# Optimization experiments

Hardware: AMD Instinct MI355X
Metric: run time of the kernel (lower is better)

## Reference

```python
import jax, jax.numpy as jnp
import numpy as np

EMBED = 1024
HIDDEN = 64  # embed_size // n_heads
B, L = 8, 4096


def setup_inputs() -> dict:
    key = jax.random.key(0)
    k1, k2, k3, k4, k5, k6, k7 = jax.random.split(key, 7)
    query = jax.random.normal(k1, (B, L, EMBED), dtype=jnp.float32)
    key_t = jax.random.normal(k2, (B, L, EMBED), dtype=jnp.float32)
    value = jax.random.normal(k3, (B, L, EMBED), dtype=jnp.float32)
    mask = jax.random.randint(k4, (B, L, L), 0, 2).astype(jnp.bool_)
    # nn.Linear(embed, hidden, bias=False) weights have shape (hidden, embed)
    s = 1.0 / np.sqrt(EMBED)
    WQ = jax.random.uniform(k5, (HIDDEN, EMBED), jnp.float32, -s, s)
    WK = jax.random.uniform(k6, (HIDDEN, EMBED), jnp.float32, -s, s)
    WV = jax.random.uniform(k7, (HIDDEN, EMBED), jnp.float32, -s, s)
    return {"query": query, "key": key_t, "value": value, "mask": mask,
            "WQ": WQ, "WK": WK, "WV": WV}


def reference(query, key, value, mask, WQ, WK, WV):
    # Projections: y = x @ W.T  (Linear without bias)
    Q = jnp.einsum('ble,he->blh', query, WQ)   # [B,L,H]
    K = jnp.einsum('ble,he->blh', key, WK)
    V = jnp.einsum('ble,he->blh', value, WV)
    scale = 1.0 / jnp.sqrt(jnp.asarray(Q.shape[-1], Q.dtype))
    scores = jnp.einsum('bqh,bkh->bqk', Q, K) * scale   # [B,L,L]
    scores = jnp.where(mask, -jnp.inf, scores)
    attn = jax.nn.softmax(scores, axis=-1)
    # dropout p=0.0 -> identity
    return jnp.einsum('bqk,bkh->bqh', attn, V)           # [B,L,H]
```

## Files before the change

### kernel.cpp

```cpp
#include <hip/hip_runtime.h>
#include <hip/hip_bf16.h>

#define NB 8
#define LL 4096
#define EE 1024
#define HH 64

typedef unsigned short u16;
typedef unsigned char u8;
typedef unsigned int u32;
typedef unsigned long long u64;
using bf16x8 = __attribute__((ext_vector_type(8))) short;
using f32x4  = __attribute__((ext_vector_type(4))) float;

__device__ __forceinline__ short f2bf(float f) {
    __hip_bfloat16 h = __float2bfloat16(f);
    return __builtin_bit_cast(short, h);
}

__device__ __forceinline__ bf16x8 pack8(const float4 a, const float4 b) {
    bf16x8 r;
    r[0] = f2bf(a.x); r[1] = f2bf(a.y); r[2] = f2bf(a.z); r[3] = f2bf(a.w);
    r[4] = f2bf(b.x); r[5] = f2bf(b.y); r[6] = f2bf(b.z); r[7] = f2bf(b.w);
    return r;
}

__global__ __launch_bounds__(256) void proj_kernel(
    const float* __restrict__ Xq, const float* __restrict__ Xk, const float* __restrict__ Xv,
    const float* __restrict__ Wq, const float* __restrict__ Wk, const float* __restrict__ Wv,
    u16* __restrict__ Oq, u16* __restrict__ Ok, u16* __restrict__ Ovt)
{
    __shared__ u16 Xs[2][64][72];
    __shared__ u16 Ws2[2][64][72];

    const int which = blockIdx.y;
    const float* X = (which == 0) ? Xq : (which == 1) ? Xk : Xv;
    const float* W = (which == 0) ? Wq : (which == 1) ? Wk : Wv;
    const float scale = (which == 0) ? 0.125f : 1.0f;

    const int tid  = threadIdx.x;
    const int lane = tid & 63;
    const int w    = tid >> 6;
    const int g    = lane >> 4;
    const int c    = lane & 15;
    const int m0   = blockIdx.x * 64;
    const int r    = tid >> 2;
    const int cb   = (tid & 3) * 16;

    const float* xrow = X + (size_t)(m0 + r) * EE + cb;
    const float* wrow = W + (size_t)r * EE + cb;

    float4 xr[4], wr[4];
    #pragma unroll
    for (int i = 0; i < 4; ++i) {
        xr[i] = reinterpret_cast<const float4*>(xrow)[i];
        wr[i] = reinterpret_cast<const float4*>(wrow)[i];
    }
    *reinterpret_cast<bf16x8*>(&Xs[0][r][cb])      = pack8(xr[0], xr[1]);
    *reinterpret_cast<bf16x8*>(&Xs[0][r][cb + 8])  = pack8(xr[2], xr[3]);
    *reinterpret_cast<bf16x8*>(&Ws2[0][r][cb])     = pack8(wr[0], wr[1]);
    *reinterpret_cast<bf16x8*>(&Ws2[0][r][cb + 8]) = pack8(wr[2], wr[3]);
    __syncthreads();

    f32x4 acc[4];
    #pragma unroll
    for (int t = 0; t < 4; ++t) acc[t] = (f32x4){0.f, 0.f, 0.f, 0.f};

    for (int s = 0; s < 16; ++s) {
        const int curb = s & 1, nxtb = curb ^ 1;
        if (s < 15) {
            #pragma unroll
            for (int i = 0; i < 4; ++i) {
                xr[i] = reinterpret_cast<const float4*>(xrow + (s + 1) * 64)[i];
                wr[i] = reinterpret_cast<const float4*>(wrow + (s + 1) * 64)[i];
            }
        }
        __builtin_amdgcn_s_setprio(1);
        #pragma unroll
        for (int kk = 0; kk < 2; ++kk) {
            bf16x8 a = *reinterpret_cast<const bf16x8*>(&Xs[curb][16*w + c][kk*32 + 8*g]);
            #pragma unroll
            for (int t = 0; t < 4; ++t) {
                bf16x8 bb = *reinterpret_cast<const bf16x8*>(&Ws2[curb][16*t + c][kk*32 + 8*g]);
                acc[t] = __builtin_amdgcn_mfma_f32_16x16x32_bf16(a, bb, acc[t], 0, 0, 0);
            }
        }
        __builtin_amdgcn_s_setprio(0);
        if (s < 15) {
            *reinterpret_cast<bf16x8*>(&Xs[nxtb][r][cb])      = pack8(xr[0], xr[1]);
            *reinterpret_cast<bf16x8*>(&Xs[nxtb][r][cb + 8])  = pack8(xr[2], xr[3]);
            *reinterpret_cast<bf16x8*>(&Ws2[nxtb][r][cb])     = pack8(wr[0], wr[1]);
            *reinterpret_cast<bf16x8*>(&Ws2[nxtb][r][cb + 8]) = pack8(wr[2], wr[3]);
        }
        __syncthreads();
    }

    if (which < 2) {
        u16* O = (which == 0) ? Oq : Ok;
        #pragma unroll
        for (int t = 0; t < 4; ++t)
            #pragma unroll
            for (int q = 0; q < 4; ++q) {
                const int mrow = m0 + 16*w + 4*g + q;
                O[(size_t)mrow * HH + 16*t + c] = (u16)f2bf(acc[t][q] * scale);
            }
    } else {
        const int bidx = m0 >> 12;
        #pragma unroll
        for (int t = 0; t < 4; ++t)
            #pragma unroll
            for (int q = 0; q < 4; ++q) {
                const int l = (m0 & (LL - 1)) + 16*w + 4*g + q;
                Ovt[((size_t)bidx * HH + 16*t + c) * LL + l] = (u16)f2bf(acc[t][q]);
            }
    }
}

__global__ __launch_bounds__(256) void attn_kernel(
    const u16* __restrict__ Qb, const u16* __restrict__ Kb, const u16* __restrict__ Vt,
    const int* __restrict__ mask, float* __restrict__ out)
{
    __shared__ u16 Ks[2][64][72];
    __shared__ u16 Vts[2][64][72];
    __shared__ u16 Ps[4][16][72];
    __shared__ u64 Pnl[2][4][64];

    const int b    = blockIdx.x & 7;
    const int q0   = (blockIdx.x >> 3) * 64;
    const int tid  = threadIdx.x;
    const int lane = tid & 63;
    const int w    = tid >> 6;
    const int g    = lane >> 4;
    const int c    = lane & 15;
    const int r    = tid >> 2;
    const int cb   = (tid & 3) * 16;
    const int mrr  = tid >> 4;
    const int mcc  = tid & 15;

    const u16* kbase = Kb + (size_t)b * LL * HH;
    const u16* vbase = Vt + (size_t)b * HH * LL;
    const int* mbase0 = mask + (size_t)b * LL * LL + (size_t)(q0 + mrr) * LL + mcc * 16;

    bf16x8 qf[2];
    {
        const u16* qp = Qb + ((size_t)b * LL + q0 + 16*w + c) * HH;
        qf[0] = *reinterpret_cast<const bf16x8*>(qp + 8*g);
        qf[1] = *reinterpret_cast<const bf16x8*>(qp + 32 + 8*g);
    }

    bf16x8 kra, krb, vra, vrb;
    int4 mA0, mA1, mA2, mA3, mB0, mB1, mB2, mB3;

    #define LOADKV(kt_) do {                                                   \
        kra = *reinterpret_cast<const bf16x8*>(kbase + (size_t)((kt_)*64 + r) * HH + cb);       \
        krb = *reinterpret_cast<const bf16x8*>(kbase + (size_t)((kt_)*64 + r) * HH + cb + 8);   \
        vra = *reinterpret_cast<const bf16x8*>(vbase + (size_t)r * LL + (kt_)*64 + cb);         \
        vrb = *reinterpret_cast<const bf16x8*>(vbase + (size_t)r * LL + (kt_)*64 + cb + 8);     \
    } while (0)
    #define WRITEKV(buf_) do {                                                 \
        *reinterpret_cast<bf16x8*>(&Ks[buf_][r][cb])      = kra;               \
        *reinterpret_cast<bf16x8*>(&Ks[buf_][r][cb + 8])  = krb;               \
        *reinterpret_cast<bf16x8*>(&Vts[buf_][r][cb])     = vra;               \
        *reinterpret_cast<bf16x8*>(&Vts[buf_][r][cb + 8]) = vrb;               \
    } while (0)
    #define MLOADX(P0, P1, P2, P3, sg) do {                                    \
        const int4* _mp = reinterpret_cast<const int4*>(                       \
            mbase0 + (size_t)(16 * ((sg) & 3)) * LL + ((sg) >> 2) * 256);      \
        P0 = _mp[0]; P1 = _mp[1]; P2 = _mp[2]; P3 = _mp[3];                    \
    } while (0)
    #define MPACKX(P0, P1, P2, P3, sg) do {                                    \
        u32 _bb =  (u32)(P0.x != 0)        | ((u32)(P0.y != 0) << 1)           \
                | ((u32)(P0.z != 0) << 2)  | ((u32)(P0.w != 0) << 3)           \
                | ((u32)(P1.x != 0) << 4)  | ((u32)(P1.y != 0) << 5)           \
                | ((u32)(P1.z != 0) << 6)  | ((u32)(P1.w != 0) << 7)           \
                | ((u32)(P2.x != 0) << 8)  | ((u32)(P2.y != 0) << 9)           \
                | ((u32)(P2.z != 0) << 10) | ((u32)(P2.w != 0) << 11)          \
                | ((u32)(P3.x != 0) << 12) | ((u32)(P3.y != 0) << 13)          \
                | ((u32)(P3.z != 0) << 14) | ((u32)(P3.w != 0) << 15);         \
        ((u16*)&Pnl[((sg) >> 2) & 1][mcc >> 2][16 * ((sg) & 3) + mrr])[mcc & 3] = (u16)_bb; \
    } while (0)

    f32x4 acc[4];
    float lpart[4];
    #pragma unroll
    for (int t = 0; t < 4; ++t) acc[t] = (f32x4){0.f, 0.f, 0.f, 0.f};
    #pragma unroll
    for (int q = 0; q < 4; ++q) lpart[q] = 0.f;

    #define TILE_BODY(CUR, PB, TI) do {                                        \
        f32x4 s[4];                                                            \
        __builtin_amdgcn_s_setprio(1);                                         \
        _Pragma("unroll")                                                      \
        for (int t = 0; t < 4; ++t) {                                          \
            s[t] = (f32x4){0.f, 0.f, 0.f, 0.f};                                \
            _Pragma("unroll")                                                  \
            for (int kk = 0; kk < 2; ++kk) {                                   \
                bf16x8 bfr = *reinterpret_cast<const bf16x8*>(&Ks[CUR][16*t + c][kk*32 + 8*g]); \
                s[t] = __builtin_amdgcn_mfma_f32_16x16x32_bf16(qf[kk], bfr, s[t], 0, 0, 0);     \
            }                                                                  \
        }                                                                      \
        __builtin_amdgcn_s_setprio(0);                                         \
        u64 mw0 = Pnl[PB][TI][16*w + 4*g + 0];                                 \
        u64 mw1 = Pnl[PB][TI][16*w + 4*g + 1];                                 \
        u64 mw2 = Pnl[PB][TI][16*w + 4*g + 2];                                 \
        u64 mw3 = Pnl[PB][TI][16*w + 4*g + 3];                                 \
        u32 mlo[4], mhi[4];                                                    \
        mlo[0] = (u32)mw0; mhi[0] = (u32)(mw0 >> 32);                          \
        mlo[1] = (u32)mw1; mhi[1] = (u32)(mw1 >> 32);                          \
        mlo[2] = (u32)mw2; mhi[2] = (u32)(mw2 >> 32);                          \
        mlo[3] = (u32)mw3; mhi[3] = (u32)(mw3 >> 32);                          \
        _Pragma("unroll")                                                      \
        for (int t = 0; t < 4; ++t)                                            \
            _Pragma("unroll")                                                  \
            for (int q = 0; q < 4; ++q) {                                      \
                u32 wsel = (t < 2) ? mlo[q] : mhi[q];                          \
                u32 bit = (wsel >> ((t & 1) * 16 + c)) & 1u;                   \
                float p = bit ? 0.f : __expf(s[t][q]);                         \
                lpart[q] += p;                                                 \
                Ps[w][4*g + q][16*t + c] = (u16)f2bf(p);                       \
            }                                                                  \
        __builtin_amdgcn_s_setprio(1);                                         \
        _Pragma("unroll")                                                      \
        for (int kk = 0; kk < 2; ++kk) {                                       \
            bf16x8 pa = *reinterpret_cast<const bf16x8*>(&Ps[w][c][kk*32 + 8*g]);               \
            _Pragma("unroll")                                                  \
            for (int t = 0; t < 4; ++t) {                                      \
                bf16x8 vfr = *reinterpret_cast<const bf16x8*>(&Vts[CUR][16*t + c][kk*32 + 8*g]);\
                acc[t] = __builtin_amdgcn_mfma_f32_16x16x32_bf16(pa, vfr, acc[t], 0, 0, 0);     \
            }                                                                  \
        }                                                                      \
        __builtin_amdgcn_s_setprio(0);                                         \
    } while (0)

    LOADKV(0);
    MLOADX(mA0, mA1, mA2, mA3, 0); MPACKX(mA0, mA1, mA2, mA3, 0);
    MLOADX(mA0, mA1, mA2, mA3, 1); MPACKX(mA0, mA1, mA2, mA3, 1);
    MLOADX(mA0, mA1, mA2, mA3, 2); MPACKX(mA0, mA1, mA2, mA3, 2);
    MLOADX(mA0, mA1, mA2, mA3, 3); MPACKX(mA0, mA1, mA2, mA3, 3);
    MLOADX(mB0, mB1, mB2, mB3, 4);
    WRITEKV(0);
    __syncthreads();

    for (int it = 0; it < 32; ++it) {
        const int f0 = 2 * it;
        const int f1 = f0 + 1;

        LOADKV(f0 + 1);
        if (f0 <= 58) MLOADX(mA0, mA1, mA2, mA3, f0 + 5);
        TILE_BODY(0, (f0 >> 2) & 1, f0 & 3);
        WRITEKV(1);
        if (f0 <= 59) MPACKX(mB0, mB1, mB2, mB3, f0 + 4);
        __syncthreads();

        if (f1 <= 62) LOADKV(f1 + 1);
        if (f1 <= 58) MLOADX(mB0, mB1, mB2, mB3, f1 + 5);
        TILE_BODY(1, (f1 >> 2) & 1, f1 & 3);
        if (f1 <= 62) WRITEKV(0);
        if (f1 <= 59) MPACKX(mA0, mA1, mA2, mA3, f1 + 4);
        __syncthreads();
    }

    #pragma unroll
    for (int off = 8; off >= 1; off >>= 1)
        #pragma unroll
        for (int q = 0; q < 4; ++q)
            lpart[q] += __shfl_xor(lpart[q], off, 64);
    #pragma unroll
    for (int q = 0; q < 4; ++q) {
        const float inv = 1.0f / lpart[q];
        const size_t row = (size_t)b * LL + q0 + 16*w + 4*g + q;
        #pragma unroll
        for (int t = 0; t < 4; ++t)
            out[row * HH + 16*t + c] = acc[t][q] * inv;
    }
}

extern "C" void kernel_launch(void* const* d_in, const int* in_sizes, int n_in,
                              void* d_out, int out_size, void* d_ws, size_t ws_size,
                              hipStream_t stream) {
    const float* query = (const float*)d_in[0];
    const float* key_t = (const float*)d_in[1];
    const float* value = (const float*)d_in[2];
    const int*   mask  = (const int*)d_in[3];
    const float* WQ    = (const float*)d_in[4];
    const float* WK    = (const float*)d_in[5];
    const float* WV    = (const float*)d_in[6];
    float* out = (float*)d_out;

    const size_t nqkv = (size_t)NB * LL * HH;
    u16* Qb  = (u16*)d_ws;
    u16* Kb  = Qb + nqkv;
    u16* Vtb = Kb + nqkv;

    dim3 pgrid(NB * LL / 64, 3);
    proj_kernel<<<pgrid, 256, 0, stream>>>(query, key_t, value, WQ, WK, WV, Qb, Kb, Vtb);

    attn_kernel<<<NB * LL / 64, 256, 0, stream>>>(Qb, Kb, Vtb, mask, out);
}
```

Before: 223.9 us.

## Read K/V MFMA fragments directly from global memory and batch mask windows

Removes the shared-memory staging of K and V tiles. Each lane now loads its MFMA B-fragments straight from global/L2, and K/V are no longer double-buffered through LDS. The main loop is restructured to process four tiles per mask window with one barrier per window instead of one per tile, which cuts synchronisation and LDS traffic. In exchange, each of the four waves fetches the same K/V fragments redundantly from global memory, and load latency is exposed inside the compute body with no explicit prefetch.

```diff
diff --git a/kernel.cpp b/kernel.cpp
--- a/kernel.cpp
+++ b/kernel.cpp
@@ -120,8 +120,6 @@
     const u16* __restrict__ Qb, const u16* __restrict__ Kb, const u16* __restrict__ Vt,
     const int* __restrict__ mask, float* __restrict__ out)
 {
-    __shared__ u16 Ks[2][64][72];
-    __shared__ u16 Vts[2][64][72];
     __shared__ u16 Ps[4][16][72];
     __shared__ u64 Pnl[2][4][64];
 
@@ -132,13 +130,11 @@
     const int w    = tid >> 6;
     const int g    = lane >> 4;
     const int c    = lane & 15;
-    const int r    = tid >> 2;
-    const int cb   = (tid & 3) * 16;
     const int mrr  = tid >> 4;
     const int mcc  = tid & 15;
 
-    const u16* kbase = Kb + (size_t)b * LL * HH;
-    const u16* vbase = Vt + (size_t)b * HH * LL;
+    const u16* kq = Kb + (size_t)b * LL * HH + (size_t)c * HH + 8 * g;
+    const u16* vq = Vt + (size_t)b * HH * LL + (size_t)c * LL + 8 * g;
     const int* mbase0 = mask + (size_t)b * LL * LL + (size_t)(q0 + mrr) * LL + mcc * 16;
 
     bf16x8 qf[2];
@@ -148,27 +144,14 @@
         qf[1] = *reinterpret_cast<const bf16x8*>(qp + 32 + 8*g);
     }
 
-    bf16x8 kra, krb, vra, vrb;
     int4 mA0, mA1, mA2, mA3, mB0, mB1, mB2, mB3;
 
-    #define LOADKV(kt_) do {                                                   \
-        kra = *reinterpret_cast<const bf16x8*>(kbase + (size_t)((kt_)*64 + r) * HH + cb);       \
-        krb = *reinterpret_cast<const bf16x8*>(kbase + (size_t)((kt_)*64 + r) * HH + cb + 8);   \
-        vra = *reinterpret_cast<const bf16x8*>(vbase + (size_t)r * LL + (kt_)*64 + cb);         \
-        vrb = *reinterpret_cast<const bf16x8*>(vbase + (size_t)r * LL + (kt_)*64 + cb + 8);     \
-    } while (0)
-    #define WRITEKV(buf_) do {                                                 \
-        *reinterpret_cast<bf16x8*>(&Ks[buf_][r][cb])      = kra;               \
-        *reinterpret_cast<bf16x8*>(&Ks[buf_][r][cb + 8])  = krb;               \
-        *reinterpret_cast<bf16x8*>(&Vts[buf_][r][cb])     = vra;               \
-        *reinterpret_cast<bf16x8*>(&Vts[buf_][r][cb + 8]) = vrb;               \
-    } while (0)
-    #define MLOADX(P0, P1, P2, P3, sg) do {                                    \
+    #define MLOADX(P0, P1, P2, P3, win_, p_) do {                              \
         const int4* _mp = reinterpret_cast<const int4*>(                       \
-            mbase0 + (size_t)(16 * ((sg) & 3)) * LL + ((sg) >> 2) * 256);      \
+            mbase0 + (size_t)(16 * (p_)) * LL + (win_) * 256);                 \
         P0 = _mp[0]; P1 = _mp[1]; P2 = _mp[2]; P3 = _mp[3];                    \
     } while (0)
-    #define MPACKX(P0, P1, P2, P3, sg) do {                                    \
+    #define MPACKX(P0, P1, P2, P3, win_, p_) do {                              \
         u32 _bb =  (u32)(P0.x != 0)        | ((u32)(P0.y != 0) << 1)           \
                 | ((u32)(P0.z != 0) << 2)  | ((u32)(P0.w != 0) << 3)           \
                 | ((u32)(P1.x != 0) << 4)  | ((u32)(P1.y != 0) << 5)           \
@@ -177,7 +160,7 @@
                 | ((u32)(P2.z != 0) << 10) | ((u32)(P2.w != 0) << 11)          \
                 | ((u32)(P3.x != 0) << 12) | ((u32)(P3.y != 0) << 13)          \
                 | ((u32)(P3.z != 0) << 14) | ((u32)(P3.w != 0) << 15);         \
-        ((u16*)&Pnl[((sg) >> 2) & 1][mcc >> 2][16 * ((sg) & 3) + mrr])[mcc & 3] = (u16)_bb; \
+        ((u16*)&Pnl[(win_) & 1][mcc >> 2][16 * (p_) + mrr])[mcc & 3] = (u16)_bb; \
     } while (0)
 
     f32x4 acc[4];
@@ -187,7 +170,7 @@
     #pragma unroll
     for (int q = 0; q < 4; ++q) lpart[q] = 0.f;
 
-    #define TILE_BODY(CUR, PB, TI) do {                                        \
+    #define TILE_BODY(TILE, PB, TI) do {                                       \
         f32x4 s[4];                                                            \
         __builtin_amdgcn_s_setprio(1);                                         \
         _Pragma("unroll")                                                      \
@@ -195,7 +178,8 @@
             s[t] = (f32x4){0.f, 0.f, 0.f, 0.f};                                \
             _Pragma("unroll")                                                  \
             for (int kk = 0; kk < 2; ++kk) {                                   \
-                bf16x8 bfr = *reinterpret_cast<const bf16x8*>(&Ks[CUR][16*t + c][kk*32 + 8*g]); \
+                bf16x8 bfr = *reinterpret_cast<const bf16x8*>(                 \
+                    kq + (TILE) * 4096 + t * 1024 + kk * 32);                  \
                 s[t] = __builtin_amdgcn_mfma_f32_16x16x32_bf16(qf[kk], bfr, s[t], 0, 0, 0);     \
             }                                                                  \
         }                                                                      \
@@ -225,38 +209,45 @@
             bf16x8 pa = *reinterpret_cast<const bf16x8*>(&Ps[w][c][kk*32 + 8*g]);               \
             _Pragma("unroll")                                                  \
             for (int t = 0; t < 4; ++t) {                                      \
-                bf16x8 vfr = *reinterpret_cast<const bf16x8*>(&Vts[CUR][16*t + c][kk*32 + 8*g]);\
+                bf16x8 vfr = *reinterpret_cast<const bf16x8*>(                 \
+                    vq + (size_t)t * 16 * LL + (TILE) * 64 + kk * 32);         \
                 acc[t] = __builtin_amdgcn_mfma_f32_16x16x32_bf16(pa, vfr, acc[t], 0, 0, 0);     \
             }                                                                  \
         }                                                                      \
         __builtin_amdgcn_s_setprio(0);                                         \
     } while (0)
 
-    LOADKV(0);
-    MLOADX(mA0, mA1, mA2, mA3, 0); MPACKX(mA0, mA1, mA2, mA3, 0);
-    MLOADX(mA0, mA1, mA2, mA3, 1); MPACKX(mA0, mA1, mA2, mA3, 1);
-    MLOADX(mA0, mA1, mA2, mA3, 2); MPACKX(mA0, mA1, mA2, mA3, 2);
-    MLOADX(mA0, mA1, mA2, mA3, 3); MPACKX(mA0, mA1, mA2, mA3, 3);
-    MLOADX(mB0, mB1, mB2, mB3, 4);
-    WRITEKV(0);
+    MLOADX(mA0, mA1, mA2, mA3, 0, 0); MPACKX(mA0, mA1, mA2, mA3, 0, 0);
+    MLOADX(mA0, mA1, mA2, mA3, 0, 1); MPACKX(mA0, mA1, mA2, mA3, 0, 1);
+    MLOADX(mA0, mA1, mA2, mA3, 0, 2); MPACKX(mA0, mA1, mA2, mA3, 0, 2);
+    MLOADX(mA0, mA1, mA2, mA3, 0, 3); MPACKX(mA0, mA1, mA2, mA3, 0, 3);
     __syncthreads();
 
-    for (int it = 0; it < 32; ++it) {
-        const int f0 = 2 * it;
-        const int f1 = f0 + 1;
-
-        LOADKV(f0 + 1);
-        if (f0 <= 58) MLOADX(mA0, mA1, mA2, mA3, f0 + 5);
-        TILE_BODY(0, (f0 >> 2) & 1, f0 & 3);
-        WRITEKV(1);
-        if (f0 <= 59) MPACKX(mB0, mB1, mB2, mB3, f0 + 4);
-        __syncthreads();
-
-        if (f1 <= 62) LOADKV(f1 + 1);
-        if (f1 <= 58) MLOADX(mB0, mB1, mB2, mB3, f1 + 5);
-        TILE_BODY(1, (f1 >> 2) & 1, f1 & 3);
-        if (f1 <= 62) WRITEKV(0);
-        if (f1 <= 59) MPACKX(mA0, mA1, mA2, mA3, f1 + 4);
+    for (int win = 0; win < 16; ++win) {
+        const int cur = win & 1;
+        const int base = 4 * win;
+        const bool more = (win + 1 < 16);
+
+        if (more) {
+            MLOADX(mA0, mA1, mA2, mA3, win + 1, 0);
+            MLOADX(mB0, mB1, mB2, mB3, win + 1, 1);
+        }
+        TILE_BODY(base + 0, cur, 0);
+        TILE_BODY(base + 1, cur, 1);
+        if (more) {
+            MPACKX(mA0, mA1, mA2, mA3, win + 1, 0);
+            MLOADX(mA0, mA1, mA2, mA3, win + 1, 2);
+        }
+        TILE_BODY(base + 2, cur, 2);
+        if (more) {
+            MPACKX(mB0, mB1, mB2, mB3, win + 1, 1);
+            MLOADX(mB0, mB1, mB2, mB3, win + 1, 3);
+        }
+        TILE_BODY(base + 3, cur, 3);
+        if (more) {
+            MPACKX(mA0, mA1, mA2, mA3, win + 1, 2);
+            MPACKX(mB0, mB1, mB2, mB3, win + 1, 3);
+        }
         __syncthreads();
     }
 
```

Result: slower. 428.6 us (+91.5%).
